# Optimization experiments

Measured on AMD Instinct MI355X. Metric: run time of the kernel, lower is better.

## Reference

```python
import jax, jax.numpy as jnp
import numpy as np

D_MODEL = 768
N_HEADS = 12
D_FF = 3072
D_K = D_MODEL // N_HEADS


def _layernorm(x, gamma, beta, eps=1e-5):
    mu = jnp.mean(x, axis=-1, keepdims=True)
    var = jnp.var(x, axis=-1, keepdims=True)
    return (x - mu) * jax.lax.rsqrt(var + eps) * gamma + beta


def setup_inputs() -> dict:
    key = jax.random.key(0)
    ks = jax.random.split(key, 16)
    B, S = 2, 2048
    s = 1.0 / np.sqrt(D_MODEL)
    inp = {
        "x": jax.random.normal(ks[0], (B, S, D_MODEL), jnp.float32),
        "mask": jnp.ones((B, 1, 1, S), jnp.int32),
        "wq": jax.random.normal(ks[1], (D_MODEL, D_MODEL), jnp.float32) * s,
        "bq": jnp.zeros((D_MODEL,), jnp.float32),
        "wk": jax.random.normal(ks[2], (D_MODEL, D_MODEL), jnp.float32) * s,
        "bk": jnp.zeros((D_MODEL,), jnp.float32),
        "wv": jax.random.normal(ks[3], (D_MODEL, D_MODEL), jnp.float32) * s,
        "bv": jnp.zeros((D_MODEL,), jnp.float32),
        "wo": jax.random.normal(ks[4], (D_MODEL, D_MODEL), jnp.float32) * s,
        "bo": jnp.zeros((D_MODEL,), jnp.float32),
        "w1": jax.random.normal(ks[5], (D_MODEL, D_FF), jnp.float32) * s,
        "b1": jnp.zeros((D_FF,), jnp.float32),
        "w2": jax.random.normal(ks[6], (D_FF, D_MODEL), jnp.float32) / np.sqrt(D_FF),
        "b2": jnp.zeros((D_MODEL,), jnp.float32),
        "g1": jnp.ones((D_MODEL,), jnp.float32),
        "be1": jnp.zeros((D_MODEL,), jnp.float32),
        "g2": jnp.ones((D_MODEL,), jnp.float32),
        "be2": jnp.zeros((D_MODEL,), jnp.float32),
    }
    return inp


def reference(x, mask, wq, bq, wk, bk, wv, bv, wo, bo, w1, b1, w2, b2, g1, be1, g2, be2):
    B, S, _ = x.shape
    # QKV projections, split into heads: [B, H, S, d_k]
    q = (x @ wq + bq).reshape(B, S, N_HEADS, D_K).transpose(0, 2, 1, 3)
    k = (x @ wk + bk).reshape(B, S, N_HEADS, D_K).transpose(0, 2, 1, 3)
    v = (x @ wv + bv).reshape(B, S, N_HEADS, D_K).transpose(0, 2, 1, 3)
    # [B, H, S, S]
    scores = jnp.einsum('bhqd,bhkd->bhqk', q, k) / np.sqrt(D_K).astype(np.float32)
    scores = jnp.where(mask == 0, -1e9, scores)
    attn = jax.nn.softmax(scores, axis=-1)  # dropout is identity in eval
    ctx = jnp.einsum('bhqk,bhkd->bhqd', attn, v)
    ctx = ctx.transpose(0, 2, 1, 3).reshape(B, S, D_MODEL)
    attn_out = ctx @ wo + bo
    x = _layernorm(x + attn_out, g1, be1)
    ff = jax.nn.gelu(x @ w1 + b1, approximate=False) @ w2 + b2
    x = _layernorm(x + ff, g2, be2)
    return x
```

## Files before the change

### kernel.cpp

```cpp
#include <hip/hip_runtime.h>
#include <hip/hip_bf16.h>
#include <math.h>

#define D_MODEL 768
#define N_HEADS 12
#define D_FF    3072
#define D_K     64
#define SEQ     2048
#define BATCH   2
#define M_TOK   (BATCH * SEQ)
#define D_QKV   (3 * D_MODEL)
#define BH      (BATCH * N_HEADS)

typedef __attribute__((ext_vector_type(8))) short short8;
typedef __attribute__((ext_vector_type(4))) float f32x4;

static __device__ __forceinline__ short f2bf(float f) {
    __hip_bfloat16 b = __float2bfloat16(f);
    return __builtin_bit_cast(short, b);
}

static __device__ __forceinline__ float gelu_f(float v) {
    const float u = 0.7978845608f * (v + 0.044715f * v * v * v);
    const float e = __expf(2.0f * u);
    const float t = 1.0f - 2.0f / (e + 1.0f);
    return 0.5f * v * (1.0f + t);
}

static __device__ __forceinline__ void load_lds16(const void* g, void* l) {
    __builtin_amdgcn_global_load_lds(
        (const __attribute__((address_space(1))) unsigned int*)g,
        (__attribute__((address_space(3))) unsigned int*)l,
        16, 0, 0);
}

__global__ __launch_bounds__(256) void prep_kernel(
    const float* __restrict__ x,  short* __restrict__ xb,
    const float* __restrict__ wq, const float* __restrict__ wk,
    const float* __restrict__ wv, short* __restrict__ wqkv_t,
    const float* __restrict__ wo, short* __restrict__ wo_t,
    const float* __restrict__ w1, short* __restrict__ w1_t,
    const float* __restrict__ w2, short* __restrict__ w2_t,
    const float* __restrict__ bq, const float* __restrict__ bk,
    const float* __restrict__ bv, float* __restrict__ bqkv)
{
    __shared__ float tile[32][33];
    const int bid = blockIdx.x;
    const int tid = threadIdx.x;

    if (bid < 6912) {
        const float* in; short* outp; int K, N, t;
        if (bid < 576)       { in = wq; outp = wqkv_t;              K = 768;  N = 768;  t = bid; }
        else if (bid < 1152) { in = wk; outp = wqkv_t + 589824;     K = 768;  N = 768;  t = bid - 576; }
        else if (bid < 1728) { in = wv; outp = wqkv_t + 2 * 589824; K = 768;  N = 768;  t = bid - 1152; }
        else if (bid < 2304) { in = wo; outp = wo_t;                K = 768;  N = 768;  t = bid - 1728; }
        else if (bid < 4608) { in = w1; outp = w1_t;                K = 768;  N = 3072; t = bid - 2304; }
        else                 { in = w2; outp = w2_t;                K = 3072; N = 768;  t = bid - 4608; }
        const int nb = N >> 5;
        const int bx = t % nb, by = t / nb;
        const int n0 = bx * 32, k0 = by * 32;
        const int tx = tid & 31, ty = tid >> 5;
#pragma unroll
        for (int i = 0; i < 32; i += 8)
            tile[ty + i][tx] = in[(size_t)(k0 + ty + i) * N + n0 + tx];
        __syncthreads();
#pragma unroll
        for (int i = 0; i < 32; i += 8)
            outp[(size_t)(n0 + ty + i) * K + k0 + tx] = f2bf(tile[tx][ty + i]);
    } else if (bid < 8448) {
        const int t = (bid - 6912) * 256 + tid;
        const float4 a = reinterpret_cast<const float4*>(x)[2 * t];
        const float4 b = reinterpret_cast<const float4*>(x)[2 * t + 1];
        short8 s;
        s[0] = f2bf(a.x); s[1] = f2bf(a.y); s[2] = f2bf(a.z); s[3] = f2bf(a.w);
        s[4] = f2bf(b.x); s[5] = f2bf(b.y); s[6] = f2bf(b.z); s[7] = f2bf(b.w);
        reinterpret_cast<short8*>(xb)[t] = s;
    } else {
        const int t = (bid - 8448) * 256 + tid;
        if (t < D_QKV)
            bqkv[t] = (t < 768) ? bq[t] : (t < 1536) ? bk[t - 768] : bv[t - 1536];
    }
}

#define EPI_QKV     0
#define EPI_GELU_BF 1
#define EPI_RES_F32 2

template <int EPI>
__global__ __launch_bounds__(256) void gemm_mfma(
    const short* __restrict__ A,
    const short* __restrict__ Bt,
    const float* __restrict__ bias,
    const float* __restrict__ res,
    void* __restrict__ Cout, void* __restrict__ Out2, void* __restrict__ Out3,
    int M, int N, int K)
{
    __shared__ short As[128 * 64];
    __shared__ short Bs[128 * 64];

    const int tid  = threadIdx.x;
    const int w    = tid >> 6;
    const int lane = tid & 63;
    const int m16  = lane & 15;
    const int quad = lane >> 4;
    const int wm   = w >> 1;
    const int wn   = w & 1;
    const int bm = blockIdx.y * 128;
    const int bn = blockIdx.x * 128;

    const int l8 = lane >> 3;
    const int scol = ((lane & 7) ^ l8) * 8;
    const int rx = m16 & 7;

    f32x4 acc[4][4];
#pragma unroll
    for (int mt = 0; mt < 4; ++mt)
#pragma unroll
        for (int nt = 0; nt < 4; ++nt)
            acc[mt][nt] = (f32x4){0.f, 0.f, 0.f, 0.f};

    for (int k0 = 0; k0 < K; k0 += 64) {
        __syncthreads();
#pragma unroll
        for (int i = 0; i < 4; ++i) {
            const int g = w * 4 + i;
            const int row = g * 8 + l8;
            load_lds16(&A [(size_t)(bm + row) * K + k0 + scol], &As[g * 512]);
            load_lds16(&Bt[(size_t)(bn + row) * K + k0 + scol], &Bs[g * 512]);
        }
        __syncthreads();

#pragma unroll
        for (int s = 0; s < 2; ++s) {
            const int cs = ((s * 4 + quad) ^ rx) * 8;
            short8 af[4], bf[4];
#pragma unroll
            for (int mt = 0; mt < 4; ++mt)
                af[mt] = *reinterpret_cast<const short8*>(
                    &As[(wm * 64 + mt * 16 + m16) * 64 + cs]);
#pragma unroll
            for (int nt = 0; nt < 4; ++nt)
                bf[nt] = *reinterpret_cast<const short8*>(
                    &Bs[(wn * 64 + nt * 16 + m16) * 64 + cs]);
#pragma unroll
            for (int mt = 0; mt < 4; ++mt)
#pragma unroll
                for (int nt = 0; nt < 4; ++nt)
                    acc[mt][nt] = __builtin_amdgcn_mfma_f32_16x16x32_bf16(
                        af[mt], bf[nt], acc[mt][nt], 0, 0, 0);
        }
    }

#pragma unroll
    for (int mt = 0; mt < 4; ++mt) {
#pragma unroll
        for (int r = 0; r < 4; ++r) {
            const int row = bm + wm * 64 + mt * 16 + quad * 4 + r;
#pragma unroll
            for (int nt = 0; nt < 4; ++nt) {
                const int col = bn + wn * 64 + nt * 16 + m16;
                float v = acc[mt][nt][r] + bias[col];
                if (EPI == EPI_QKV) {
                    const int b = row >> 11;
                    const int s = row & 2047;
                    const int sec = (col >= 1536) ? 2 : (col >= 768) ? 1 : 0;
                    const int cm = col - sec * 768;
                    const int h = cm >> 6;
                    const int d = cm & 63;
                    const int bh = b * N_HEADS + h;
                    if (sec == 0) {
                        ((short*)Cout)[((size_t)bh * SEQ + s) * 64 + d] = f2bf(v * 0.125f);
                    } else if (sec == 1) {
                        ((short*)Out2)[((size_t)bh * SEQ + s) * 64 + d] = f2bf(v);
                    } else {
                        ((short*)Out3)[((size_t)bh * 64 + d) * SEQ + s] = f2bf(v);
                    }
                } else if (EPI == EPI_GELU_BF) {
                    ((short*)Cout)[(size_t)row * N + col] = f2bf(gelu_f(v));
                } else {
                    v += res[(size_t)row * N + col];
                    ((float*)Cout)[(size_t)row * N + col] = v;
                }
            }
        }
    }
}

template <int EPI>
__global__ __launch_bounds__(256) void gemm_bn64(
    const short* __restrict__ A, const short* __restrict__ Bt,
    const float* __restrict__ bias, const float* __restrict__ res,
    void* __restrict__ Cout, int M, int N, int K)
{
    __shared__ short As[128 * 64];
    __shared__ short Bs[64 * 64];

    const int tid  = threadIdx.x;
    const int w    = tid >> 6;
    const int lane = tid & 63;
    const int m16  = lane & 15;
    const int quad = lane >> 4;
    const int bm = blockIdx.y * 128;
    const int bn = blockIdx.x * 64;

    const int l8 = lane >> 3;
    const int scol = ((lane & 7) ^ l8) * 8;
    const int rx = m16 & 7;

    f32x4 acc[2][4];
#pragma unroll
    for (int mt = 0; mt < 2; ++mt)
#pragma unroll
        for (int nt = 0; nt < 4; ++nt)
            acc[mt][nt] = (f32x4){0.f, 0.f, 0.f, 0.f};

    for (int k0 = 0; k0 < K; k0 += 64) {
        __syncthreads();
#pragma unroll
        for (int i = 0; i < 4; ++i) {
            const int g = w * 4 + i;
            load_lds16(&A[(size_t)(bm + g * 8 + l8) * K + k0 + scol], &As[g * 512]);
        }
#pragma unroll
        for (int i = 0; i < 2; ++i) {
            const int g = w * 2 + i;
            load_lds16(&Bt[(size_t)(bn + g * 8 + l8) * K + k0 + scol], &Bs[g * 512]);
        }
        __syncthreads();

#pragma unroll
        for (int s = 0; s < 2; ++s) {
            const int cs = ((s * 4 + quad) ^ rx) * 8;
            short8 af[2], bf[4];
#pragma unroll
            for (int mt = 0; mt < 2; ++mt)
                af[mt] = *reinterpret_cast<const short8*>(
                    &As[(w * 32 + mt * 16 + m16) * 64 + cs]);
#pragma unroll
            for (int nt = 0; nt < 4; ++nt)
                bf[nt] = *reinterpret_cast<const short8*>(
                    &Bs[(nt * 16 + m16) * 64 + cs]);
#pragma unroll
            for (int mt = 0; mt < 2; ++mt)
#pragma unroll
                for (int nt = 0; nt < 4; ++nt)
                    acc[mt][nt] = __builtin_amdgcn_mfma_f32_16x16x32_bf16(
                        af[mt], bf[nt], acc[mt][nt], 0, 0, 0);
        }
    }

#pragma unroll
    for (int mt = 0; mt < 2; ++mt) {
#pragma unroll
        for (int r = 0; r < 4; ++r) {
            const int row = bm + w * 32 + mt * 16 + quad * 4 + r;
#pragma unroll
            for (int nt = 0; nt < 4; ++nt) {
                const int col = bn + nt * 16 + m16;
                float v = acc[mt][nt][r] + bias[col];
                if (EPI == EPI_RES_F32) {
                    v += res[(size_t)row * N + col];
                    ((float*)Cout)[(size_t)row * N + col] = v;
                } else {
                    ((short*)Cout)[(size_t)row * N + col] = f2bf(v);
                }
            }
        }
    }
}

#define KT 128
#define PSTR 136

__global__ __launch_bounds__(256) void attn_mfma_kernel(
    const short* __restrict__ qb, const short* __restrict__ kb,
    const short* __restrict__ vtb, const int* __restrict__ mask,
    short* __restrict__ ctx)
{
    __shared__ short Klds[KT * 64];
    __shared__ short Vtlds[D_K * KT];
    __shared__ short Plds[4 * 16 * PSTR];

    const int tid  = threadIdx.x;
    const int lane = tid & 63;
    const int wv   = tid >> 6;
    const int m16  = lane & 15;
    const int quad = lane >> 4;

    const int qtile = blockIdx.x * 64;
    const int bh = blockIdx.y;
    const int b = bh / N_HEADS;

    const size_t qrow = (size_t)bh * SEQ + qtile + wv * 16 + m16;
    short8 qf[2];
#pragma unroll
    for (int kc = 0; kc < 2; ++kc)
        qf[kc] = *reinterpret_cast<const short8*>(
            &qb[qrow * 64 + kc * 32 + quad * 8]);

    short8 ones;
#pragma unroll
    for (int i = 0; i < 8; ++i) ones[i] = (short)0x3F80;

    f32x4 o[4];
#pragma unroll
    for (int nt = 0; nt < 4; ++nt) o[nt] = (f32x4){0.f, 0.f, 0.f, 0.f};
    f32x4 lacc = (f32x4){0.f, 0.f, 0.f, 0.f};

    const int* mrow = mask + (size_t)b * SEQ;

    const int l8 = lane >> 3;
    const int kcol = ((lane & 7) ^ l8) * 8;
    const int l16 = lane >> 4;
    const int c16 = lane & 15;
    const int rx8 = m16 & 7;

    for (int kt0 = 0; kt0 < SEQ; kt0 += KT) {
        __syncthreads();
#pragma unroll
        for (int i = 0; i < 4; ++i) {
            const int g = wv * 4 + i;
            const int row = g * 8 + l8;
            load_lds16(&kb[((size_t)bh * SEQ + kt0 + row) * 64 + kcol], &Klds[g * 512]);
        }
#pragma unroll
        for (int i = 0; i < 4; ++i) {
            const int g = wv * 4 + i;
            const int row = g * 4 + l16;
            const int vcol = (c16 ^ (row & 15)) * 8;
            load_lds16(&vtb[((size_t)bh * 64 + row) * SEQ + kt0 + vcol], &Vtlds[g * 512]);
        }
        __syncthreads();

        f32x4 s[8];
#pragma unroll
        for (int nt = 0; nt < 8; ++nt) s[nt] = (f32x4){0.f, 0.f, 0.f, 0.f};
#pragma unroll
        for (int nt = 0; nt < 8; ++nt) {
#pragma unroll
            for (int kc = 0; kc < 2; ++kc) {
                const short8 kf = *reinterpret_cast<const short8*>(
                    &Klds[(nt * 16 + m16) * 64 + (((kc * 4 + quad) ^ rx8) * 8)]);
                s[nt] = __builtin_amdgcn_mfma_f32_16x16x32_bf16(qf[kc], kf, s[nt], 0, 0, 0);
            }
        }

        short* Pw = &Plds[wv * 16 * PSTR];
#pragma unroll
        for (int nt = 0; nt < 8; ++nt) {
            const int mk = mrow[kt0 + nt * 16 + m16];
#pragma unroll
            for (int r = 0; r < 4; ++r) {
                const float sv = (mk == 0) ? -1e9f : fminf(s[nt][r], 30.f);
                Pw[(quad * 4 + r) * PSTR + nt * 16 + m16] = f2bf(__expf(sv));
            }
        }

#pragma unroll
        for (int kc = 0; kc < 4; ++kc) {
            const short8 af = *reinterpret_cast<const short8*>(
                &Pw[m16 * PSTR + kc * 32 + quad * 8]);
#pragma unroll
            for (int nt = 0; nt < 4; ++nt) {
                const short8 bf = *reinterpret_cast<const short8*>(
                    &Vtlds[(nt * 16 + m16) * KT + (((kc * 4 + quad) ^ m16) * 8)]);
                o[nt] = __builtin_amdgcn_mfma_f32_16x16x32_bf16(af, bf, o[nt], 0, 0, 0);
            }
            lacc = __builtin_amdgcn_mfma_f32_16x16x32_bf16(af, ones, lacc, 0, 0, 0);
        }
    }

    const int h = bh % N_HEADS;
#pragma unroll
    for (int r = 0; r < 4; ++r) {
        const float inv_l = 1.0f / lacc[r];
        const size_t row = (size_t)(b * SEQ + qtile + wv * 16 + quad * 4 + r);
#pragma unroll
        for (int nt = 0; nt < 4; ++nt)
            ctx[row * D_MODEL + h * D_K + nt * 16 + m16] = f2bf(o[nt][r] * inv_l);
    }
}

template <bool DUAL>
__global__ __launch_bounds__(256) void layernorm_kernel(
    const float* __restrict__ in, const float* __restrict__ g,
    const float* __restrict__ be, float* __restrict__ outf,
    short* __restrict__ outb)
{
    const int row = blockIdx.x;
    const float* x = in + (size_t)row * D_MODEL;

    float s = 0.0f, s2 = 0.0f;
    for (int i = threadIdx.x; i < D_MODEL; i += 256) {
        const float v = x[i];
        s += v; s2 += v * v;
    }
#pragma unroll
    for (int off = 32; off > 0; off >>= 1) {
        s  += __shfl_down(s, off);
        s2 += __shfl_down(s2, off);
    }
    __shared__ float red[2][4];
    const int wid = threadIdx.x >> 6;
    const int lane = threadIdx.x & 63;
    if (lane == 0) { red[0][wid] = s; red[1][wid] = s2; }
    __syncthreads();
    __shared__ float stats[2];
    if (threadIdx.x == 0) {
        float ts = 0.0f, ts2 = 0.0f;
#pragma unroll
        for (int w = 0; w < 4; ++w) { ts += red[0][w]; ts2 += red[1][w]; }
        const float mu = ts * (1.0f / D_MODEL);
        const float var = ts2 * (1.0f / D_MODEL) - mu * mu;
        stats[0] = mu;
        stats[1] = rsqrtf(var + 1e-5f);
    }
    __syncthreads();
    const float mu = stats[0], rstd = stats[1];
    for (int i = threadIdx.x; i < D_MODEL; i += 256) {
        const float v = (x[i] - mu) * rstd * g[i] + be[i];
        outf[(size_t)row * D_MODEL + i] = v;
        if (DUAL) outb[(size_t)row * D_MODEL + i] = f2bf(v);
    }
}

extern "C" void kernel_launch(void* const* d_in, const int* in_sizes, int n_in,
                              void* d_out, int out_size, void* d_ws, size_t ws_size,
                              hipStream_t stream)
{
    const float* x    = (const float*)d_in[0];
    const int*   mask = (const int*)  d_in[1];
    const float* wq   = (const float*)d_in[2];
    const float* bq   = (const float*)d_in[3];
    const float* wk   = (const float*)d_in[4];
    const float* bk   = (const float*)d_in[5];
    const float* wv   = (const float*)d_in[6];
    const float* bv   = (const float*)d_in[7];
    const float* wo   = (const float*)d_in[8];
    const float* bo   = (const float*)d_in[9];
    const float* w1   = (const float*)d_in[10];
    const float* b1   = (const float*)d_in[11];
    const float* w2   = (const float*)d_in[12];
    const float* b2   = (const float*)d_in[13];
    const float* g1   = (const float*)d_in[14];
    const float* be1  = (const float*)d_in[15];
    const float* g2   = (const float*)d_in[16];
    const float* be2  = (const float*)d_in[17];

    float* out = (float*)d_out;

    char* cur = (char*)d_ws;
    auto alloc = [&](size_t bytes) { char* p = cur; cur += (bytes + 255) & ~(size_t)255; return p; };

    short* xb      = (short*)alloc((size_t)M_TOK * D_MODEL * 2);
    short* qbuf    = (short*)alloc((size_t)BH * SEQ * D_K * 2);
    short* kbuf    = (short*)alloc((size_t)BH * SEQ * D_K * 2);
    short* vtbuf   = (short*)alloc((size_t)BH * D_K * SEQ * 2);
    short* ctxb    = (short*)alloc((size_t)M_TOK * D_MODEL * 2);
    short* x1b     = (short*)alloc((size_t)M_TOK * D_MODEL * 2);
    short* ffb     = (short*)alloc((size_t)M_TOK * D_FF * 2);
    short* wqkv_t  = (short*)alloc((size_t)D_QKV * D_MODEL * 2);
    short* wo_t    = (short*)alloc((size_t)D_MODEL * D_MODEL * 2);
    short* w1_t    = (short*)alloc((size_t)D_FF * D_MODEL * 2);
    short* w2_t    = (short*)alloc((size_t)D_MODEL * D_FF * 2);
    float* bqkv    = (float*)alloc((size_t)D_QKV * 4);
    float* h1      = (float*)alloc((size_t)M_TOK * D_MODEL * 4);
    float* x1f     = (float*)alloc((size_t)M_TOK * D_MODEL * 4);
    float* h2      = (float*)alloc((size_t)M_TOK * D_MODEL * 4);

    const dim3 blk(256);

    hipLaunchKernelGGL(prep_kernel, dim3(8457), blk, 0, stream,
                       x, xb, wq, wk, wv, wqkv_t, wo, wo_t,
                       w1, w1_t, w2, w2_t, bq, bk, bv, bqkv);

    hipLaunchKernelGGL((gemm_mfma<EPI_QKV>), dim3(D_QKV / 128, M_TOK / 128), blk, 0, stream,
                       xb, wqkv_t, bqkv, nullptr, qbuf, kbuf, vtbuf, M_TOK, D_QKV, D_MODEL);

    hipLaunchKernelGGL(attn_mfma_kernel, dim3(SEQ / 64, BH), blk, 0, stream,
                       qbuf, kbuf, vtbuf, mask, ctxb);

    hipLaunchKernelGGL((gemm_bn64<EPI_RES_F32>), dim3(D_MODEL / 64, M_TOK / 128), blk, 0, stream,
                       ctxb, wo_t, bo, x, h1, M_TOK, D_MODEL, D_MODEL);

    hipLaunchKernelGGL((layernorm_kernel<true>), dim3(M_TOK), blk, 0, stream,
                       h1, g1, be1, x1f, x1b);

    hipLaunchKernelGGL((gemm_mfma<EPI_GELU_BF>), dim3(D_FF / 128, M_TOK / 128), blk, 0, stream,
                       x1b, w1_t, b1, nullptr, ffb, nullptr, nullptr, M_TOK, D_FF, D_MODEL);

    hipLaunchKernelGGL((gemm_bn64<EPI_RES_F32>), dim3(D_MODEL / 64, M_TOK / 128), blk, 0, stream,
                       ffb, w2_t, b2, x1f, h2, M_TOK, D_MODEL, D_FF);

    hipLaunchKernelGGL((layernorm_kernel<false>), dim3(M_TOK), blk, 0, stream,
                       h2, g2, be2, out, nullptr);
}
```

Before: 320.1 us.

## Double-buffer LDS tiles in MFMA GEMMs to overlap global loads with compute

Both bf16 MFMA GEMM kernels now keep two LDS buffers per operand. The next K-tile is issued with global_load_lds while the current tile is consumed, and a vmcnt wait counts only the just-issued loads as outstanding. This replaces the load-then-sync-then-compute pattern, so global memory latency is meant to hide behind MFMA work. It doubles LDS use per block, which may lower occupancy, and it depends on hand-set waitcnt counts and sched barriers being right.

```diff
diff --git a/kernel.cpp b/kernel.cpp
--- a/kernel.cpp
+++ b/kernel.cpp
@@ -33,6 +33,8 @@
         (__attribute__((address_space(3))) unsigned int*)l,
         16, 0, 0);
 }
+
+#define WAITCNT_VM(N) (0xF70 | (N))
 
 __global__ __launch_bounds__(256) void prep_kernel(
     const float* __restrict__ x,  short* __restrict__ xb,
@@ -95,8 +97,8 @@
     void* __restrict__ Cout, void* __restrict__ Out2, void* __restrict__ Out3,
     int M, int N, int K)
 {
-    __shared__ short As[128 * 64];
-    __shared__ short Bs[128 * 64];
+    __shared__ short As[2][128 * 64];
+    __shared__ short Bs[2][128 * 64];
 
     const int tid  = threadIdx.x;
     const int w    = tid >> 6;
@@ -112,24 +114,35 @@
     const int scol = ((lane & 7) ^ l8) * 8;
     const int rx = m16 & 7;
 
-    f32x4 acc[4][4];
-#pragma unroll
-    for (int mt = 0; mt < 4; ++mt)
-#pragma unroll
-        for (int nt = 0; nt < 4; ++nt)
-            acc[mt][nt] = (f32x4){0.f, 0.f, 0.f, 0.f};
-
-    for (int k0 = 0; k0 < K; k0 += 64) {
-        __syncthreads();
+    auto stage = [&](int k0, int buf) {
 #pragma unroll
         for (int i = 0; i < 4; ++i) {
             const int g = w * 4 + i;
             const int row = g * 8 + l8;
-            load_lds16(&A [(size_t)(bm + row) * K + k0 + scol], &As[g * 512]);
-            load_lds16(&Bt[(size_t)(bn + row) * K + k0 + scol], &Bs[g * 512]);
-        }
-        __syncthreads();
-
+            load_lds16(&A [(size_t)(bm + row) * K + k0 + scol], &As[buf][g * 512]);
+            load_lds16(&Bt[(size_t)(bn + row) * K + k0 + scol], &Bs[buf][g * 512]);
+        }
+    };
+
+    f32x4 acc[4][4];
+#pragma unroll
+    for (int mt = 0; mt < 4; ++mt)
+#pragma unroll
+        for (int nt = 0; nt < 4; ++nt)
+            acc[mt][nt] = (f32x4){0.f, 0.f, 0.f, 0.f};
+
+    const int niter = K >> 6;
+    stage(0, 0);
+
+    int it = 0;
+    for (; it < niter - 1; ++it) {
+        const int cur = it & 1;
+        __builtin_amdgcn_sched_barrier(0);
+        __builtin_amdgcn_s_barrier();
+        stage((it + 1) << 6, cur ^ 1);
+        __builtin_amdgcn_s_waitcnt(WAITCNT_VM(8));
+        __builtin_amdgcn_s_barrier();
+        __builtin_amdgcn_sched_barrier(0);
 #pragma unroll
         for (int s = 0; s < 2; ++s) {
             const int cs = ((s * 4 + quad) ^ rx) * 8;
@@ -137,11 +150,36 @@
 #pragma unroll
             for (int mt = 0; mt < 4; ++mt)
                 af[mt] = *reinterpret_cast<const short8*>(
-                    &As[(wm * 64 + mt * 16 + m16) * 64 + cs]);
+                    &As[cur][(wm * 64 + mt * 16 + m16) * 64 + cs]);
 #pragma unroll
             for (int nt = 0; nt < 4; ++nt)
                 bf[nt] = *reinterpret_cast<const short8*>(
-                    &Bs[(wn * 64 + nt * 16 + m16) * 64 + cs]);
+                    &Bs[cur][(wn * 64 + nt * 16 + m16) * 64 + cs]);
+#pragma unroll
+            for (int mt = 0; mt < 4; ++mt)
+#pragma unroll
+                for (int nt = 0; nt < 4; ++nt)
+                    acc[mt][nt] = __builtin_amdgcn_mfma_f32_16x16x32_bf16(
+                        af[mt], bf[nt], acc[mt][nt], 0, 0, 0);
+        }
+    }
+    {
+        const int cur = it & 1;
+        __builtin_amdgcn_s_waitcnt(WAITCNT_VM(0));
+        __builtin_amdgcn_s_barrier();
+        __builtin_amdgcn_sched_barrier(0);
+#pragma unroll
+        for (int s = 0; s < 2; ++s) {
+            const int cs = ((s * 4 + quad) ^ rx) * 8;
+            short8 af[4], bf[4];
+#pragma unroll
+            for (int mt = 0; mt < 4; ++mt)
+                af[mt] = *reinterpret_cast<const short8*>(
+                    &As[cur][(wm * 64 + mt * 16 + m16) * 64 + cs]);
+#pragma unroll
+            for (int nt = 0; nt < 4; ++nt)
+                bf[nt] = *reinterpret_cast<const short8*>(
+                    &Bs[cur][(wn * 64 + nt * 16 + m16) * 64 + cs]);
 #pragma unroll
             for (int mt = 0; mt < 4; ++mt)
 #pragma unroll
@@ -192,8 +230,8 @@
     const float* __restrict__ bias, const float* __restrict__ res,
     void* __restrict__ Cout, int M, int N, int K)
 {
-    __shared__ short As[128 * 64];
-    __shared__ short Bs[64 * 64];
+    __shared__ short As[2][128 * 64];
+    __shared__ short Bs[2][64 * 64];
 
     const int tid  = threadIdx.x;
     const int w    = tid >> 6;
@@ -207,6 +245,19 @@
     const int scol = ((lane & 7) ^ l8) * 8;
     const int rx = m16 & 7;
 
+    auto stage = [&](int k0, int buf) {
+#pragma unroll
+        for (int i = 0; i < 4; ++i) {
+            const int g = w * 4 + i;
+            load_lds16(&A[(size_t)(bm + g * 8 + l8) * K + k0 + scol], &As[buf][g * 512]);
+        }
+#pragma unroll
+        for (int i = 0; i < 2; ++i) {
+            const int g = w * 2 + i;
+            load_lds16(&Bt[(size_t)(bn + g * 8 + l8) * K + k0 + scol], &Bs[buf][g * 512]);
+        }
+    };
+
     f32x4 acc[2][4];
 #pragma unroll
     for (int mt = 0; mt < 2; ++mt)
@@ -214,20 +265,18 @@
         for (int nt = 0; nt < 4; ++nt)
             acc[mt][nt] = (f32x4){0.f, 0.f, 0.f, 0.f};
 
-    for (int k0 = 0; k0 < K; k0 += 64) {
-        __syncthreads();
-#pragma unroll
-        for (int i = 0; i < 4; ++i) {
-            const int g = w * 4 + i;
-            load_lds16(&A[(size_t)(bm + g * 8 + l8) * K + k0 + scol], &As[g * 512]);
-        }
-#pragma unroll
-        for (int i = 0; i < 2; ++i) {
-            const int g = w * 2 + i;
-            load_lds16(&Bt[(size_t)(bn + g * 8 + l8) * K + k0 + scol], &Bs[g * 512]);
-        }
-        __syncthreads();
-
+    const int niter = K >> 6;
+    stage(0, 0);
+
+    int it = 0;
+    for (; it < niter - 1; ++it) {
+        const int cur = it & 1;
+        __builtin_amdgcn_sched_barrier(0);
+        __builtin_amdgcn_s_barrier();
+        stage((it + 1) << 6, cur ^ 1);
+        __builtin_amdgcn_s_waitcnt(WAITCNT_VM(6));
+        __builtin_amdgcn_s_barrier();
+        __builtin_amdgcn_sched_barrier(0);
 #pragma unroll
         for (int s = 0; s < 2; ++s) {
             const int cs = ((s * 4 + quad) ^ rx) * 8;
@@ -235,11 +284,36 @@
 #pragma unroll
             for (int mt = 0; mt < 2; ++mt)
                 af[mt] = *reinterpret_cast<const short8*>(
-                    &As[(w * 32 + mt * 16 + m16) * 64 + cs]);
+                    &As[cur][(w * 32 + mt * 16 + m16) * 64 + cs]);
 #pragma unroll
             for (int nt = 0; nt < 4; ++nt)
                 bf[nt] = *reinterpret_cast<const short8*>(
-                    &Bs[(nt * 16 + m16) * 64 + cs]);
+                    &Bs[cur][(nt * 16 + m16) * 64 + cs]);
+#pragma unroll
+            for (int mt = 0; mt < 2; ++mt)
+#pragma unroll
+                for (int nt = 0; nt < 4; ++nt)
+                    acc[mt][nt] = __builtin_amdgcn_mfma_f32_16x16x32_bf16(
+                        af[mt], bf[nt], acc[mt][nt], 0, 0, 0);
+        }
+    }
+    {
+        const int cur = it & 1;
+        __builtin_amdgcn_s_waitcnt(WAITCNT_VM(0));
+        __builtin_amdgcn_s_barrier();
+        __builtin_amdgcn_sched_barrier(0);
+#pragma unroll
+        for (int s = 0; s < 2; ++s) {
+            const int cs = ((s * 4 + quad) ^ rx) * 8;
+            short8 af[2], bf[4];
+#pragma unroll
+            for (int mt = 0; mt < 2; ++mt)
+                af[mt] = *reinterpret_cast<const short8*>(
+                    &As[cur][(w * 32 + mt * 16 + m16) * 64 + cs]);
+#pragma unroll
+            for (int nt = 0; nt < 4; ++nt)
+                bf[nt] = *reinterpret_cast<const short8*>(
+                    &Bs[cur][(nt * 16 + m16) * 64 + cs]);
 #pragma unroll
             for (int mt = 0; mt < 2; ++mt)
 #pragma unroll
```

Result: no change. 316.3 us (-1.2%).

## Double-buffer LDS loads in GEMMs and attention, unify GEMMs on 128x64 tiles

Applied to the files above, without the earlier changes.

Merges the two GEMM kernels into one 128x64-tile kernel that double-buffers A/B tiles in LDS. It issues the next tile's global-to-LDS loads before computing on the current tile, with explicit waitcnt and barriers. The attention kernel gets the same double-buffering with the key tile shrunk from 128 to 64 and the mask staged once into LDS. The goal is to overlap memory latency with MFMA work, at the cost of smaller tiles (less reuse per block for the QKV and FF1 GEMMs) and more LDS per block.

```diff
diff --git a/kernel.cpp b/kernel.cpp
--- a/kernel.cpp
+++ b/kernel.cpp
@@ -33,6 +33,8 @@
         (__attribute__((address_space(3))) unsigned int*)l,
         16, 0, 0);
 }
+
+#define WAITCNT_VM(N) (0xF70 | (N))
 
 __global__ __launch_bounds__(256) void prep_kernel(
     const float* __restrict__ x,  short* __restrict__ xb,
@@ -87,7 +89,7 @@
 #define EPI_RES_F32 2
 
 template <int EPI>
-__global__ __launch_bounds__(256) void gemm_mfma(
+__global__ __launch_bounds__(256) void gemm64(
     const short* __restrict__ A,
     const short* __restrict__ Bt,
     const float* __restrict__ bias,
@@ -95,55 +97,70 @@
     void* __restrict__ Cout, void* __restrict__ Out2, void* __restrict__ Out3,
     int M, int N, int K)
 {
-    __shared__ short As[128 * 64];
-    __shared__ short Bs[128 * 64];
+    __shared__ short As[2][128 * 64];
+    __shared__ short Bs[2][64 * 64];
 
     const int tid  = threadIdx.x;
     const int w    = tid >> 6;
     const int lane = tid & 63;
     const int m16  = lane & 15;
     const int quad = lane >> 4;
-    const int wm   = w >> 1;
-    const int wn   = w & 1;
     const int bm = blockIdx.y * 128;
-    const int bn = blockIdx.x * 128;
+    const int bn = blockIdx.x * 64;
 
     const int l8 = lane >> 3;
     const int scol = ((lane & 7) ^ l8) * 8;
     const int rx = m16 & 7;
 
-    f32x4 acc[4][4];
-#pragma unroll
-    for (int mt = 0; mt < 4; ++mt)
+    auto stage = [&](int k0, int buf) {
+#pragma unroll
+        for (int i = 0; i < 4; ++i) {
+            const int g = w * 4 + i;
+            load_lds16(&A[(size_t)(bm + g * 8 + l8) * K + k0 + scol], &As[buf][g * 512]);
+        }
+#pragma unroll
+        for (int i = 0; i < 2; ++i) {
+            const int g = w * 2 + i;
+            load_lds16(&Bt[(size_t)(bn + g * 8 + l8) * K + k0 + scol], &Bs[buf][g * 512]);
+        }
+    };
+
+    f32x4 acc[2][4];
+#pragma unroll
+    for (int mt = 0; mt < 2; ++mt)
 #pragma unroll
         for (int nt = 0; nt < 4; ++nt)
             acc[mt][nt] = (f32x4){0.f, 0.f, 0.f, 0.f};
 
-    for (int k0 = 0; k0 < K; k0 += 64) {
-        __syncthreads();
-#pragma unroll
-        for (int i = 0; i < 4; ++i) {
-            const int g = w * 4 + i;
-            const int row = g * 8 + l8;
-            load_lds16(&A [(size_t)(bm + row) * K + k0 + scol], &As[g * 512]);
-            load_lds16(&Bt[(size_t)(bn + row) * K + k0 + scol], &Bs[g * 512]);
-        }
-        __syncthreads();
-
+    const int niter = K >> 6;
+    stage(0, 0);
+
+    for (int it = 0; it < niter; ++it) {
+        const int cur = it & 1;
+        __builtin_amdgcn_sched_barrier(0);
+        __builtin_amdgcn_s_barrier();
+        if (it + 1 < niter) {
+            stage((it + 1) << 6, cur ^ 1);
+            __builtin_amdgcn_s_waitcnt(WAITCNT_VM(6));
+        } else {
+            __builtin_amdgcn_s_waitcnt(WAITCNT_VM(0));
+        }
+        __builtin_amdgcn_s_barrier();
+        __builtin_amdgcn_sched_barrier(0);
 #pragma unroll
         for (int s = 0; s < 2; ++s) {
             const int cs = ((s * 4 + quad) ^ rx) * 8;
-            short8 af[4], bf[4];
-#pragma unroll
-            for (int mt = 0; mt < 4; ++mt)
+            short8 af[2], bf[4];
+#pragma unroll
+            for (int mt = 0; mt < 2; ++mt)
                 af[mt] = *reinterpret_cast<const short8*>(
-                    &As[(wm * 64 + mt * 16 + m16) * 64 + cs]);
+                    &As[cur][(w * 32 + mt * 16 + m16) * 64 + cs]);
 #pragma unroll
             for (int nt = 0; nt < 4; ++nt)
                 bf[nt] = *reinterpret_cast<const short8*>(
-                    &Bs[(wn * 64 + nt * 16 + m16) * 64 + cs]);
-#pragma unroll
-            for (int mt = 0; mt < 4; ++mt)
+                    &Bs[cur][(nt * 16 + m16) * 64 + cs]);
+#pragma unroll
+            for (int mt = 0; mt < 2; ++mt)
 #pragma unroll
                 for (int nt = 0; nt < 4; ++nt)
                     acc[mt][nt] = __builtin_amdgcn_mfma_f32_16x16x32_bf16(
@@ -152,13 +169,13 @@
     }
 
 #pragma unroll
-    for (int mt = 0; mt < 4; ++mt) {
+    for (int mt = 0; mt < 2; ++mt) {
 #pragma unroll
         for (int r = 0; r < 4; ++r) {
-            const int row = bm + wm * 64 + mt * 16 + quad * 4 + r;
+            const int row = bm + w * 32 + mt * 16 + quad * 4 + r;
 #pragma unroll
             for (int nt = 0; nt < 4; ++nt) {
-                const int col = bn + wn * 64 + nt * 16 + m16;
+                const int col = bn + nt * 16 + m16;
                 float v = acc[mt][nt][r] + bias[col];
                 if (EPI == EPI_QKV) {
                     const int b = row >> 11;
@@ -186,100 +203,18 @@
     }
 }
 
-template <int EPI>
-__global__ __launch_bounds__(256) void gemm_bn64(
-    const short* __restrict__ A, const short* __restrict__ Bt,
-    const float* __restrict__ bias, const float* __restrict__ res,
-    void* __restrict__ Cout, int M, int N, int K)
-{
-    __shared__ short As[128 * 64];
-    __shared__ short Bs[64 * 64];
-
-    const int tid  = threadIdx.x;
-    const int w    = tid >> 6;
-    const int lane = tid & 63;
-    const int m16  = lane & 15;
-    const int quad = lane >> 4;
-    const int bm = blockIdx.y * 128;
-    const int bn = blockIdx.x * 64;
-
-    const int l8 = lane >> 3;
-    const int scol = ((lane & 7) ^ l8) * 8;
-    const int rx = m16 & 7;
-
-    f32x4 acc[2][4];
-#pragma unroll
-    for (int mt = 0; mt < 2; ++mt)
-#pragma unroll
-        for (int nt = 0; nt < 4; ++nt)
-            acc[mt][nt] = (f32x4){0.f, 0.f, 0.f, 0.f};
-
-    for (int k0 = 0; k0 < K; k0 += 64) {
-        __syncthreads();
-#pragma unroll
-        for (int i = 0; i < 4; ++i) {
-            const int g = w * 4 + i;
-            load_lds16(&A[(size_t)(bm + g * 8 + l8) * K + k0 + scol], &As[g * 512]);
-        }
-#pragma unroll
-        for (int i = 0; i < 2; ++i) {
-            const int g = w * 2 + i;
-            load_lds16(&Bt[(size_t)(bn + g * 8 + l8) * K + k0 + scol], &Bs[g * 512]);
-        }
-        __syncthreads();
-
-#pragma unroll
-        for (int s = 0; s < 2; ++s) {
-            const int cs = ((s * 4 + quad) ^ rx) * 8;
-            short8 af[2], bf[4];
-#pragma unroll
-            for (int mt = 0; mt < 2; ++mt)
-                af[mt] = *reinterpret_cast<const short8*>(
-                    &As[(w * 32 + mt * 16 + m16) * 64 + cs]);
-#pragma unroll
-            for (int nt = 0; nt < 4; ++nt)
-                bf[nt] = *reinterpret_cast<const short8*>(
-                    &Bs[(nt * 16 + m16) * 64 + cs]);
-#pragma unroll
-            for (int mt = 0; mt < 2; ++mt)
-#pragma unroll
-                for (int nt = 0; nt < 4; ++nt)
-                    acc[mt][nt] = __builtin_amdgcn_mfma_f32_16x16x32_bf16(
-                        af[mt], bf[nt], acc[mt][nt], 0, 0, 0);
-        }
-    }
-
-#pragma unroll
-    for (int mt = 0; mt < 2; ++mt) {
-#pragma unroll
-        for (int r = 0; r < 4; ++r) {
-            const int row = bm + w * 32 + mt * 16 + quad * 4 + r;
-#pragma unroll
-            for (int nt = 0; nt < 4; ++nt) {
-                const int col = bn + nt * 16 + m16;
-                float v = acc[mt][nt][r] + bias[col];
-                if (EPI == EPI_RES_F32) {
-                    v += res[(size_t)row * N + col];
-                    ((float*)Cout)[(size_t)row * N + col] = v;
-                } else {
-                    ((short*)Cout)[(size_t)row * N + col] = f2bf(v);
-                }
-            }
-        }
-    }
-}
-
-#define KT 128
-#define PSTR 136
+#define KT 64
+#define PSTR 72
 
 __global__ __launch_bounds__(256) void attn_mfma_kernel(
     const short* __restrict__ qb, const short* __restrict__ kb,
     const short* __restrict__ vtb, const int* __restrict__ mask,
     short* __restrict__ ctx)
 {
-    __shared__ short Klds[KT * 64];
-    __shared__ short Vtlds[D_K * KT];
+    __shared__ short Klds[2][KT * 64];
+    __shared__ short Vtlds[2][64 * KT];
     __shared__ short Plds[4 * 16 * PSTR];
+    __shared__ short Mlds[SEQ];
 
     const int tid  = threadIdx.x;
     const int lane = tid & 63;
@@ -298,6 +233,9 @@
         qf[kc] = *reinterpret_cast<const short8*>(
             &qb[qrow * 64 + kc * 32 + quad * 8]);
 
+    for (int i = tid; i < SEQ; i += 256)
+        Mlds[i] = (short)(mask[(size_t)b * SEQ + i] != 0);
+
     short8 ones;
 #pragma unroll
     for (int i = 0; i < 8; ++i) ones[i] = (short)0x3F80;
@@ -307,63 +245,70 @@
     for (int nt = 0; nt < 4; ++nt) o[nt] = (f32x4){0.f, 0.f, 0.f, 0.f};
     f32x4 lacc = (f32x4){0.f, 0.f, 0.f, 0.f};
 
-    const int* mrow = mask + (size_t)b * SEQ;
-
     const int l8 = lane >> 3;
     const int kcol = ((lane & 7) ^ l8) * 8;
-    const int l16 = lane >> 4;
-    const int c16 = lane & 15;
-    const int rx8 = m16 & 7;
-
-    for (int kt0 = 0; kt0 < SEQ; kt0 += KT) {
-        __syncthreads();
-#pragma unroll
-        for (int i = 0; i < 4; ++i) {
-            const int g = wv * 4 + i;
-            const int row = g * 8 + l8;
-            load_lds16(&kb[((size_t)bh * SEQ + kt0 + row) * 64 + kcol], &Klds[g * 512]);
-        }
-#pragma unroll
-        for (int i = 0; i < 4; ++i) {
-            const int g = wv * 4 + i;
-            const int row = g * 4 + l16;
-            const int vcol = (c16 ^ (row & 15)) * 8;
-            load_lds16(&vtb[((size_t)bh * 64 + row) * SEQ + kt0 + vcol], &Vtlds[g * 512]);
-        }
-        __syncthreads();
-
-        f32x4 s[8];
-#pragma unroll
-        for (int nt = 0; nt < 8; ++nt) s[nt] = (f32x4){0.f, 0.f, 0.f, 0.f};
-#pragma unroll
-        for (int nt = 0; nt < 8; ++nt) {
+    auto stage = [&](int kt0, int buf) {
+#pragma unroll
+        for (int g = 0; g < 2; ++g) {
+            const int row = g * 32 + wv * 8 + l8;
+            load_lds16(&kb [((size_t)bh * SEQ + kt0 + row) * 64 + kcol],
+                       &Klds[buf][g * 2048 + wv * 512]);
+            load_lds16(&vtb[((size_t)bh * 64 + row) * SEQ + kt0 + kcol],
+                       &Vtlds[buf][g * 2048 + wv * 512]);
+        }
+    };
+
+    __syncthreads();
+    stage(0, 0);
+
+    const int rx = m16 & 7;
+    const int NIT = SEQ / KT;
+    for (int it = 0; it < NIT; ++it) {
+        const int cur = it & 1;
+        const int kt0 = it * KT;
+        __builtin_amdgcn_sched_barrier(0);
+        __builtin_amdgcn_s_barrier();
+        if (it + 1 < NIT) {
+            stage((it + 1) * KT, cur ^ 1);
+            __builtin_amdgcn_s_waitcnt(WAITCNT_VM(4));
+        } else {
+            __builtin_amdgcn_s_waitcnt(WAITCNT_VM(0));
+        }
+        __builtin_amdgcn_s_barrier();
+        __builtin_amdgcn_sched_barrier(0);
+
+        f32x4 s[4];
+#pragma unroll
+        for (int nt = 0; nt < 4; ++nt) s[nt] = (f32x4){0.f, 0.f, 0.f, 0.f};
+#pragma unroll
+        for (int nt = 0; nt < 4; ++nt) {
 #pragma unroll
             for (int kc = 0; kc < 2; ++kc) {
                 const short8 kf = *reinterpret_cast<const short8*>(
-                    &Klds[(nt * 16 + m16) * 64 + (((kc * 4 + quad) ^ rx8) * 8)]);
+                    &Klds[cur][(nt * 16 + m16) * 64 + (((kc * 4 + quad) ^ rx) * 8)]);
                 s[nt] = __builtin_amdgcn_mfma_f32_16x16x32_bf16(qf[kc], kf, s[nt], 0, 0, 0);
             }
         }
 
         short* Pw = &Plds[wv * 16 * PSTR];
 #pragma unroll
-        for (int nt = 0; nt < 8; ++nt) {
-            const int mk = mrow[kt0 + nt * 16 + m16];
+        for (int nt = 0; nt < 4; ++nt) {
+            const short mk = Mlds[kt0 + nt * 16 + m16];
 #pragma unroll
             for (int r = 0; r < 4; ++r) {
-                const float sv = (mk == 0) ? -1e9f : fminf(s[nt][r], 30.f);
+                const float sv = mk ? fminf(s[nt][r], 30.f) : -1e9f;
                 Pw[(quad * 4 + r) * PSTR + nt * 16 + m16] = f2bf(__expf(sv));
             }
         }
 
 #pragma unroll
-        for (int kc = 0; kc < 4; ++kc) {
+        for (int kc = 0; kc < 2; ++kc) {
             const short8 af = *reinterpret_cast<const short8*>(
                 &Pw[m16 * PSTR + kc * 32 + quad * 8]);
 #pragma unroll
             for (int nt = 0; nt < 4; ++nt) {
                 const short8 bf = *reinterpret_cast<const short8*>(
-                    &Vtlds[(nt * 16 + m16) * KT + (((kc * 4 + quad) ^ m16) * 8)]);
+                    &Vtlds[cur][(nt * 16 + m16) * 64 + (((kc * 4 + quad) ^ rx) * 8)]);
                 o[nt] = __builtin_amdgcn_mfma_f32_16x16x32_bf16(af, bf, o[nt], 0, 0, 0);
             }
             lacc = __builtin_amdgcn_mfma_f32_16x16x32_bf16(af, ones, lacc, 0, 0, 0);
@@ -474,23 +419,23 @@
                        x, xb, wq, wk, wv, wqkv_t, wo, wo_t,
                        w1, w1_t, w2, w2_t, bq, bk, bv, bqkv);
 
-    hipLaunchKernelGGL((gemm_mfma<EPI_QKV>), dim3(D_QKV / 128, M_TOK / 128), blk, 0, stream,
+    hipLaunchKernelGGL((gemm64<EPI_QKV>), dim3(D_QKV / 64, M_TOK / 128), blk, 0, stream,
                        xb, wqkv_t, bqkv, nullptr, qbuf, kbuf, vtbuf, M_TOK, D_QKV, D_MODEL);
 
     hipLaunchKernelGGL(attn_mfma_kernel, dim3(SEQ / 64, BH), blk, 0, stream,
                        qbuf, kbuf, vtbuf, mask, ctxb);
 
-    hipLaunchKernelGGL((gemm_bn64<EPI_RES_F32>), dim3(D_MODEL / 64, M_TOK / 128), blk, 0, stream,
-                       ctxb, wo_t, bo, x, h1, M_TOK, D_MODEL, D_MODEL);
+    hipLaunchKernelGGL((gemm64<EPI_RES_F32>), dim3(D_MODEL / 64, M_TOK / 128), blk, 0, stream,
+                       ctxb, wo_t, bo, x, h1, nullptr, nullptr, M_TOK, D_MODEL, D_MODEL);
 
     hipLaunchKernelGGL((layernorm_kernel<true>), dim3(M_TOK), blk, 0, stream,
                        h1, g1, be1, x1f, x1b);
 
-    hipLaunchKernelGGL((gemm_mfma<EPI_GELU_BF>), dim3(D_FF / 128, M_TOK / 128), blk, 0, stream,
+    hipLaunchKernelGGL((gemm64<EPI_GELU_BF>), dim3(D_FF / 64, M_TOK / 128), blk, 0, stream,
                        x1b, w1_t, b1, nullptr, ffb, nullptr, nullptr, M_TOK, D_FF, D_MODEL);
 
-    hipLaunchKernelGGL((gemm_bn64<EPI_RES_F32>), dim3(D_MODEL / 64, M_TOK / 128), blk, 0, stream,
-                       ffb, w2_t, b2, x1f, h2, M_TOK, D_MODEL, D_FF);
+    hipLaunchKernelGGL((gemm64<EPI_RES_F32>), dim3(D_MODEL / 64, M_TOK / 128), blk, 0, stream,
+                       ffb, w2_t, b2, x1f, h2, nullptr, nullptr, M_TOK, D_MODEL, D_FF);
 
     hipLaunchKernelGGL((layernorm_kernel<false>), dim3(M_TOK), blk, 0, stream,
                        h2, g2, be2, out, nullptr);
```

New measurement: 316.7 us. About the same (-1.1%).
